# Optimization experiments

Measured on AMD Instinct MI355X. Metric: run time of the kernel, lower is better.

## Reference

```python
import jax, jax.numpy as jnp
import numpy as np

B, T, E, D, OUT = 128, 64, 256, 256, 1  # batch, timesteps, encoder_hidden, decoder_hidden, out_feats


def setup_inputs() -> dict:
    key = jax.random.key(0)
    ks = jax.random.split(key, 14)
    s = 0.05
    return {
        "input_encoded": jax.random.normal(ks[0], (B, T, E), jnp.float32),
        "y_history": jax.random.normal(ks[1], (B, T - 1, OUT), jnp.float32),
        # attn_layer: Linear(2D+E -> E), Tanh, Linear(E -> 1)
        "W_a1": jax.random.normal(ks[2], (E, 2 * D + E), jnp.float32) * s,
        "b_a1": jax.random.normal(ks[3], (E,), jnp.float32) * s,
        "W_a2": jax.random.normal(ks[4], (1, E), jnp.float32) * s,
        "b_a2": jax.random.normal(ks[5], (1,), jnp.float32) * s,
        # fc: Linear(E + out_feats -> out_feats)
        "W_fc": jax.random.normal(ks[6], (OUT, E + OUT), jnp.float32) * s,
        "b_fc": jax.random.normal(ks[7], (OUT,), jnp.float32) * s,
        # LSTM(input_size=out_feats, hidden_size=D), gate order i,f,g,o
        "W_ih": jax.random.normal(ks[8], (4 * D, OUT), jnp.float32) * s,
        "W_hh": jax.random.normal(ks[9], (4 * D, D), jnp.float32) * s,
        "b_ih": jax.random.normal(ks[10], (4 * D,), jnp.float32) * s,
        "b_hh": jax.random.normal(ks[11], (4 * D,), jnp.float32) * s,
        # fc_final: Linear(D + E -> 2) (probabilistic=True)
        "W_ff": jax.random.normal(ks[12], (2, D + E), jnp.float32) * s,
        "b_ff": jax.random.normal(ks[13], (2,), jnp.float32) * s,
    }


def reference(input_encoded, y_history, W_a1, b_a1, W_a2, b_a2, W_fc, b_fc,
              W_ih, W_hh, b_ih, b_hh, W_ff, b_ff):
    Bn, Tn, En = input_encoded.shape
    Dn = W_hh.shape[1]

    def step(carry, y_t):
        h, c, _ = carry  # h, c: [B, D]
        # concat(hidden, cell, enc) broadcast over the T encoder positions -> [B, T, 2D+E]
        feats = jnp.concatenate([
            jnp.broadcast_to(h[:, None, :], (Bn, Tn, Dn)),
            jnp.broadcast_to(c[:, None, :], (Bn, Tn, Dn)),
            input_encoded,
        ], axis=2)
        scores = jnp.tanh(feats @ W_a1.T + b_a1) @ W_a2.T + b_a2  # [B, T, 1]
        attn = jax.nn.softmax(scores[..., 0], axis=1)              # [B, T]
        context = jnp.einsum('bt,bte->be', attn, input_encoded)   # [B, E]
        y_tilde = jnp.concatenate([context, y_t], axis=1) @ W_fc.T + b_fc  # [B, 1]
        # single LSTM step, PyTorch gate order (i, f, g, o)
        gates = y_tilde @ W_ih.T + b_ih + h @ W_hh.T + b_hh       # [B, 4D]
        i, f, g, o = jnp.split(gates, 4, axis=1)
        c_new = jax.nn.sigmoid(f) * c + jax.nn.sigmoid(i) * jnp.tanh(g)
        h_new = jax.nn.sigmoid(o) * jnp.tanh(c_new)
        return (h_new, c_new, context), None

    h0 = jnp.zeros((Bn, Dn), input_encoded.dtype)
    c0 = jnp.zeros((Bn, Dn), input_encoded.dtype)
    ctx0 = jnp.zeros((Bn, En), input_encoded.dtype)
    # data_integration=True: loop runs T-1 steps over y_history
    (h, c, context), _ = jax.lax.scan(step, (h0, c0, ctx0), jnp.swapaxes(y_history, 0, 1))
    return jnp.concatenate([h, context], axis=1) @ W_ff.T + b_ff  # [B, 2]
```

## Files before the change

kernel.cpp:

```cpp
#include <hip/hip_runtime.h>
#include <math.h>

#define BATCH 128
#define TENC  64
#define NSTEP 63

#define OFF_WA1ET  0
#define OFF_EPT    65536
#define OFF_PKH    2162688
#define OFF_SX     2359296
#define OFF_HC     2375680
#define OFF_FLAGS  2441216

typedef __attribute__((ext_vector_type(8))) _Float16 h8_t;
typedef __attribute__((ext_vector_type(2))) _Float16 h2_t;

#if defined(__has_builtin)
#if __has_builtin(__builtin_amdgcn_fdot2)
#define FDOT2(a, b, c) __builtin_amdgcn_fdot2((a), (b), (c), false)
#endif
#endif
#ifndef FDOT2
#define FDOT2(a, b, c) ((c) + (float)(a)[0] * (float)(b)[0] + (float)(a)[1] * (float)(b)[1])
#endif

__device__ __forceinline__ h2_t h2of(h8_t v, int i) {
    h2_t r = {v[2 * i], v[2 * i + 1]};
    return r;
}
__device__ __forceinline__ float ftanh(float x) {
    x = fminf(15.f, fmaxf(-15.f, x));
    float e = __expf(2.f * x);
    return (e - 1.f) * __builtin_amdgcn_rcpf(e + 1.f);
}
__device__ __forceinline__ float fsig(float x) {
    return __builtin_amdgcn_rcpf(1.f + __expf(-x));
}

__global__ void pack_weights(const float* __restrict__ Wa1,
                             const float* __restrict__ Whh,
                             float* __restrict__ ws) {
    int idx = blockIdx.x * blockDim.x + threadIdx.x;
    _Float16* PKH = (_Float16*)(ws + OFF_PKH);
    if (idx < 131072) {
        int m = idx & 7, j7 = (idx >> 3) & 127, it = (idx >> 10) & 3;
        int seg = (idx >> 12) & 1, kc = (idx >> 13) & 7, hp = (idx >> 16) & 1;
        int owner = seg ? (1 - hp) : hp;
        int idx256 = kc * 32 + it * 8 + m;
        int k = (idx256 < 128) ? owner * 128 + idx256
                               : 256 + owner * 128 + (idx256 - 128);
        int j = hp * 128 + j7;
        PKH[idx] = (_Float16)Wa1[j * 768 + k];
    } else if (idx < 393216) {
        int n = idx - 131072;
        int m = n & 7, qp = (n >> 3) & 511, kh = (n >> 12) & 1, kk = (n >> 13) & 15, h1 = n >> 17;
        int q = ((qp >> 7) << 8) + h1 * 128 + (qp & 127);
        int k = kh * 128 + kk * 8 + m;
        PKH[131072 + n] = (_Float16)Whh[q * 256 + k];
    } else if (idx < 458752) {
        int n = idx - 393216;
        int k = n >> 8, j = n & 255;
        ws[OFF_WA1ET + n] = Wa1[j * 768 + 512 + k];
    }
}

__global__ void zero_flags(float* __restrict__ ws) {
    unsigned* f = (unsigned*)(ws + OFF_FLAGS);
    f[threadIdx.x] = 0u;
}

__global__ void enc_proj_kernel(const float* __restrict__ enc,
                                const float* __restrict__ ba1,
                                float* __restrict__ ws) {
    __shared__ float smem[8448];
    const int b  = blockIdx.x >> 1;
    const int th = blockIdx.x & 1;
    const int t0 = th * 32;
    const int tid = threadIdx.x;

    const float* encb = enc + (b * TENC + t0) * 256;
    for (int c = 0; c < 32; ++c) smem[c * 256 + tid] = encb[c * 256 + tid];
    __syncthreads();

    const int w = tid >> 6, l = tid & 63;
    float acc[8][4];
    #pragma unroll
    for (int a = 0; a < 8; ++a)
        #pragma unroll
        for (int c = 0; c < 4; ++c) acc[a][c] = 0.f;

    const float4* WT = (const float4*)(ws + OFF_WA1ET);
    for (int k = 0; k < 256; ++k) {
        float4 wv = WT[k * 64 + l];
        #pragma unroll
        for (int tt = 0; tt < 8; ++tt) {
            float e = smem[(w * 8 + tt) * 256 + k];
            acc[tt][0] += e * wv.x; acc[tt][1] += e * wv.y;
            acc[tt][2] += e * wv.z; acc[tt][3] += e * wv.w;
        }
    }
    float4 bb = ((const float4*)ba1)[l];
    __syncthreads();
    #pragma unroll
    for (int tt = 0; tt < 8; ++tt) {
        smem[(4 * l + 0) * 33 + w * 8 + tt] = acc[tt][0] + bb.x;
        smem[(4 * l + 1) * 33 + w * 8 + tt] = acc[tt][1] + bb.y;
        smem[(4 * l + 2) * 33 + w * 8 + tt] = acc[tt][2] + bb.z;
        smem[(4 * l + 3) * 33 + w * 8 + tt] = acc[tt][3] + bb.w;
    }
    __syncthreads();
    float* EPT = ws + OFF_EPT + b * 16384;
    for (int c = 0; c < 32; ++c) {
        int i = c * 256 + tid;
        int j = i >> 5, t5 = i & 31;
        EPT[j * 64 + t0 + t5] = smem[j * 33 + t5];
    }
}

__global__ __launch_bounds__(1024, 4) void decoder_main(
    const float* __restrict__ enc, const float* __restrict__ yhist,
    const float* __restrict__ Wa2,
    const float* __restrict__ Wfc, const float* __restrict__ bfc,
    const float* __restrict__ wih, const float* __restrict__ bih,
    const float* __restrict__ bhh,
    const float* __restrict__ Wff, const float* __restrict__ bff,
    float* __restrict__ ws, float* __restrict__ out) {

    __shared__ float hc[512];
    __shared__ _Float16 hcf16[512] __attribute__((aligned(16)));
    __shared__ float z[128];
    __shared__ float red1[1024];
    __shared__ float red2[1024];
    __shared__ float g2[1024];
    __shared__ float attnw[64];
    __shared__ float encw[64];
    __shared__ float sownl[64];
    __shared__ float wa2s[128];
    __shared__ float ys[64];
    __shared__ float ytil_s;
    __shared__ h8_t  wc[4096] __attribute__((aligned(16)));
    __shared__ float epl[8192];

    const int bid  = blockIdx.x;
    const int b    = bid & 127;
    const int h1   = bid >> 7;
    const int tid  = threadIdx.x;
    const int lane = tid & 63;
    const int wv   = tid >> 6;

    const _Float16* PKH = (const _Float16*)(ws + OFF_PKH);

    const float* EPTb = ws + OFF_EPT + b * 16384 + h1 * 8192;
    const float* encb = enc + b * 16384;
    #pragma unroll
    for (int i = 0; i < 8; ++i) epl[i * 1024 + tid] = EPTb[i * 1024 + tid];
    const h8_t* PKGown = (const h8_t*)(PKH + 131072) + h1 * 16384;
    #pragma unroll
    for (int kk = 0; kk < 4; ++kk) wc[kk * 1024 + tid] = PKGown[kk * 1024 + tid];
    if (tid < 512) { hc[tid] = 0.f; hcf16[tid] = (_Float16)0.f; }
    if (tid < 128) wa2s[tid] = Wa2[h1 * 128 + tid];
    if (tid < NSTEP) ys[tid] = yhist[b * NSTEP + tid];
    const float bfc0  = bfc[0];
    const float wfc_y = Wfc[256];
    float wii = 0.f, wif = 0.f, wig = 0.f, wio = 0.f;
    float bsi = 0.f, bsf = 0.f, bsg = 0.f, bso = 0.f;
    if (tid < 128) {
        const int q0 = h1 * 128 + tid;
        wii = wih[q0];       bsi = bih[q0]       + bhh[q0];
        wif = wih[256 + q0]; bsf = bih[256 + q0] + bhh[256 + q0];
        wig = wih[512 + q0]; bsg = bih[512 + q0] + bhh[512 + q0];
        wio = wih[768 + q0]; bso = bih[768 + q0] + bhh[768 + q0];
    }
    {
        const int t = tid >> 4, cch = tid & 15;
        float p = 0.f;
        #pragma unroll
        for (int i = 0; i < 16; ++i)
            p += encb[t * 256 + cch * 16 + i] * Wfc[cch * 16 + i];
        red1[t * 16 + cch] = p;
    }
    __syncthreads();
    if (tid < 64) {
        float s = 0.f;
        #pragma unroll
        for (int c = 0; c < 16; ++c) s += red1[tid * 16 + c];
        encw[tid] = s;
    }
    __syncthreads();

    const int kc = tid >> 7, j7 = tid & 127;
    const h8_t* W1 = (const h8_t*)PKH + h1 * 8192 + kc * 1024 + j7;
    const _Float16* hb_own  = hcf16 + ((kc < 4) ? h1 * 128 + kc * 32
                                                : 256 + h1 * 128 + (kc - 4) * 32);
    const _Float16* hb_peer = hcf16 + ((kc < 4) ? (1 - h1) * 128 + kc * 32
                                                : 256 + (1 - h1) * 128 + (kc - 4) * 32);
    const int kh = tid >> 9, qp = tid & 511;
    const h8_t* W4 = PKGown + kh * 512 + qp;
    const _Float16* hgk = hcf16 + kh * 128;

    float* SXown  = ws + OFF_SX + (b * 2 + h1) * 64;
    float* SXpeer = ws + OFF_SX + (b * 2 + (1 - h1)) * 64;
    float* HCown  = ws + OFF_HC + (b * 2 + h1) * 256;
    float* HCpeer = ws + OFF_HC + (b * 2 + (1 - h1)) * 256;
    unsigned* FLGown  = (unsigned*)(ws + OFF_FLAGS) + (b * 2 + h1) * 2;
    unsigned* FLGpeer = (unsigned*)(ws + OFF_FLAGS) + (b * 2 + (1 - h1)) * 2;

    for (int step = 0; step < NSTEP; ++step) {
        const unsigned tgt = (unsigned)(step + 1);
        float a0 = 0.f, a1 = 0.f;
        #pragma unroll
        for (int it = 0; it < 4; ++it) {
            h8_t w  = W1[it * 128];
            h8_t hv = *(const h8_t*)(hb_own + it * 8);
            a0 = FDOT2(h2of(w, 0), h2of(hv, 0), a0);
            a1 = FDOT2(h2of(w, 1), h2of(hv, 1), a1);
            a0 = FDOT2(h2of(w, 2), h2of(hv, 2), a0);
            a1 = FDOT2(h2of(w, 3), h2of(hv, 3), a1);
        }
        if (tid == 0 && step > 0) {
            while (atomicAdd(&FLGpeer[0], 0u) < (unsigned)step) { __builtin_amdgcn_s_sleep(1); }
        }
        __syncthreads();
        if (tid < 256 && step > 0) {
            float v = atomicAdd(&HCpeer[tid], 0.f);
            const int ih = (tid < 128) ? (1 - h1) * 128 + tid
                                       : 256 + (1 - h1) * 128 + (tid - 128);
            hc[ih] = v; hcf16[ih] = (_Float16)v;
        }
        __syncthreads();
        #pragma unroll
        for (int it = 0; it < 4; ++it) {
            h8_t w  = W1[512 + it * 128];
            h8_t hv = *(const h8_t*)(hb_peer + it * 8);
            a0 = FDOT2(h2of(w, 0), h2of(hv, 0), a0);
            a1 = FDOT2(h2of(w, 1), h2of(hv, 1), a1);
            a0 = FDOT2(h2of(w, 2), h2of(hv, 2), a0);
            a1 = FDOT2(h2of(w, 3), h2of(hv, 3), a1);
        }
        red1[kc * 128 + j7] = a0 + a1;
        __syncthreads();
        if (tid < 128) {
            float s = red1[tid];
            #pragma unroll
            for (int c = 1; c < 8; ++c) s += red1[c * 128 + tid];
            z[tid] = s;
        }
        __syncthreads();

        {
            const int jc = tid >> 6;
            float partial = 0.f;
            #pragma unroll
            for (int jj = 0; jj < 8; ++jj) {
                const int j = jc * 8 + jj;
                float v = epl[j * 64 + lane] + z[j];
                partial += ftanh(v) * wa2s[j];
            }
            red2[jc * 64 + lane] = partial;
        }
        __syncthreads();

        if (wv == 0) {
            float s = 0.f;
            #pragma unroll
            for (int w2 = 0; w2 < 16; ++w2) s += red2[w2 * 64 + lane];
            sownl[lane] = s;
            atomicExch(&SXown[lane], s);
            asm volatile("s_waitcnt vmcnt(0)" ::: "memory");
            if (lane == 0) atomicExch(&FLGown[1], tgt);
        }
        float g0 = 0.f, g1 = 0.f;
        #pragma unroll
        for (int kk = 0; kk < 4; ++kk) {
            h8_t w  = wc[kk * 1024 + tid];
            h8_t hv = *(const h8_t*)(hgk + kk * 8);
            g0 = FDOT2(h2of(w, 0), h2of(hv, 0), g0);
            g1 = FDOT2(h2of(w, 1), h2of(hv, 1), g1);
            g0 = FDOT2(h2of(w, 2), h2of(hv, 2), g0);
            g1 = FDOT2(h2of(w, 3), h2of(hv, 3), g1);
        }
        #pragma unroll 4
        for (int kk = 4; kk < 16; ++kk) {
            h8_t w  = W4[kk * 1024];
            h8_t hv = *(const h8_t*)(hgk + kk * 8);
            g0 = FDOT2(h2of(w, 0), h2of(hv, 0), g0);
            g1 = FDOT2(h2of(w, 1), h2of(hv, 1), g1);
            g0 = FDOT2(h2of(w, 2), h2of(hv, 2), g0);
            g1 = FDOT2(h2of(w, 3), h2of(hv, 3), g1);
        }
        g2[tid] = g0 + g1;
        if (tid == 0) {
            while (atomicAdd(&FLGpeer[1], 0u) < tgt) { __builtin_amdgcn_s_sleep(1); }
        }
        __syncthreads();

        if (wv == 0) {
            float sp = atomicAdd(&SXpeer[lane], 0.f);
            float s  = sownl[lane] + sp;
            float m = s;
            #pragma unroll
            for (int d = 32; d >= 1; d >>= 1) m = fmaxf(m, __shfl_xor(m, d));
            float e = __expf(s - m);
            float su = e;
            #pragma unroll
            for (int d = 32; d >= 1; d >>= 1) su += __shfl_xor(su, d);
            float a = e * __builtin_amdgcn_rcpf(su);
            attnw[lane] = a;
            float yp = a * encw[lane];
            #pragma unroll
            for (int d = 32; d >= 1; d >>= 1) yp += __shfl_xor(yp, d);
            if (lane == 0) ytil_s = yp + wfc_y * ys[step] + bfc0;
        }
        __syncthreads();

        if (tid < 128) {
            const float ytil = ytil_s;
            float gi = g2[tid]       + g2[512 + tid] + ytil * wii + bsi;
            float gf = g2[128 + tid] + g2[640 + tid] + ytil * wif + bsf;
            float gg = g2[256 + tid] + g2[768 + tid] + ytil * wig + bsg;
            float go = g2[384 + tid] + g2[896 + tid] + ytil * wio + bso;
            const int ih = h1 * 128 + tid;
            float co = hc[256 + ih];
            float cn = fsig(gf) * co + fsig(gi) * ftanh(gg);
            float hn = fsig(go) * ftanh(cn);
            hc[ih] = hn; hc[256 + ih] = cn;
            hcf16[ih] = (_Float16)hn; hcf16[256 + ih] = (_Float16)cn;
            atomicExch(&HCown[tid], hn);
            atomicExch(&HCown[128 + tid], cn);
        }
        __syncthreads();
        if (tid == 0) atomicExch(&FLGown[0], tgt);
    }

    if (tid == 0) {
        while (atomicAdd(&FLGpeer[0], 0u) < (unsigned)NSTEP) { __builtin_amdgcn_s_sleep(1); }
    }
    __syncthreads();
    if (tid < 128) {
        hc[(1 - h1) * 128 + tid] = atomicAdd(&HCpeer[tid], 0.f);
    }
    __syncthreads();

    if (h1 == 0) {
        if (tid < 256) {
            float cv = 0.f;
            #pragma unroll 8
            for (int t = 0; t < TENC; ++t)
                cv += attnw[t] * encb[t * 256 + tid];
            red1[tid] = cv;
        }
        __syncthreads();
        if (wv < 2) {
            float partial = 0.f;
            #pragma unroll
            for (int qq = 0; qq < 8; ++qq) {
                const int e2 = qq * 64 + lane;
                float v = (e2 < 256) ? hc[e2] : red1[e2 - 256];
                partial += v * Wff[wv * 512 + e2];
            }
            #pragma unroll
            for (int d = 32; d >= 1; d >>= 1) partial += __shfl_xor(partial, d);
            if (lane == 0) out[b * 2 + wv] = partial + bff[wv];
        }
    }
}

extern "C" void kernel_launch(void* const* d_in, const int* in_sizes, int n_in,
                              void* d_out, int out_size, void* d_ws, size_t ws_size,
                              hipStream_t stream) {
    const float* enc = (const float*)d_in[0];
    const float* yh  = (const float*)d_in[1];
    const float* Wa1 = (const float*)d_in[2];
    const float* ba1 = (const float*)d_in[3];
    const float* Wa2 = (const float*)d_in[4];
    const float* Wfc = (const float*)d_in[6];
    const float* bfc = (const float*)d_in[7];
    const float* Wih = (const float*)d_in[8];
    const float* Whh = (const float*)d_in[9];
    const float* bih = (const float*)d_in[10];
    const float* bhh = (const float*)d_in[11];
    const float* Wff = (const float*)d_in[12];
    const float* bff = (const float*)d_in[13];
    float* ws  = (float*)d_ws;
    float* out = (float*)d_out;

    hipLaunchKernelGGL(pack_weights, dim3(1792), dim3(256), 0, stream, Wa1, Whh, ws);
    hipLaunchKernelGGL(zero_flags, dim3(1), dim3(512), 0, stream, ws);
    hipLaunchKernelGGL(enc_proj_kernel, dim3(256), dim3(256), 0, stream, enc, ba1, ws);
    hipLaunchKernelGGL(decoder_main, dim3(256), dim3(1024), 0, stream,
                       enc, yh, Wa2, Wfc, bfc, Wih, bih, bhh, Wff, bff, ws, out);
}
```

Baseline: 424.2 us.

## Pack h/c exchange into fp16 pairs, cache more gate weights, drop a barrier

The cross-block exchange of h and c now packs both as fp16 into one 32-bit word, which halves the atomic global traffic per step. The two warps in the LSTM update each recompute the softmax and y_tilde themselves, so the shared scalar and one __syncthreads per step are gone. The LDS-resident portion of the recurrent weights grows from 4 to 6 chunks, which cuts global weight loads in the gate matvec. In exchange, the final h used by fc_final now carries fp16 rounding for the peer half, and the larger LDS footprint may affect occupancy.

```diff
diff --git a/kernel.cpp b/kernel.cpp
--- a/kernel.cpp
+++ b/kernel.cpp
@@ -9,8 +9,8 @@
 #define OFF_EPT    65536
 #define OFF_PKH    2162688
 #define OFF_SX     2359296
-#define OFF_HC     2375680
-#define OFF_FLAGS  2441216
+#define OFF_HX     2375680
+#define OFF_FLAGS  2408448
 
 typedef __attribute__((ext_vector_type(8))) _Float16 h8_t;
 typedef __attribute__((ext_vector_type(2))) _Float16 h2_t;
@@ -35,6 +35,11 @@
 }
 __device__ __forceinline__ float fsig(float x) {
     return __builtin_amdgcn_rcpf(1.f + __expf(-x));
+}
+__device__ __forceinline__ unsigned pack_hc(float h, float c) {
+    unsigned short hu = __builtin_bit_cast(unsigned short, (_Float16)h);
+    unsigned short cu = __builtin_bit_cast(unsigned short, (_Float16)c);
+    return (unsigned)hu | ((unsigned)cu << 16);
 }
 
 __global__ void pack_weights(const float* __restrict__ Wa1,
@@ -137,8 +142,7 @@
     __shared__ float sownl[64];
     __shared__ float wa2s[128];
     __shared__ float ys[64];
-    __shared__ float ytil_s;
-    __shared__ h8_t  wc[4096] __attribute__((aligned(16)));
+    __shared__ h8_t  wc[6144] __attribute__((aligned(16)));
     __shared__ float epl[8192];
 
     const int bid  = blockIdx.x;
@@ -156,7 +160,7 @@
     for (int i = 0; i < 8; ++i) epl[i * 1024 + tid] = EPTb[i * 1024 + tid];
     const h8_t* PKGown = (const h8_t*)(PKH + 131072) + h1 * 16384;
     #pragma unroll
-    for (int kk = 0; kk < 4; ++kk) wc[kk * 1024 + tid] = PKGown[kk * 1024 + tid];
+    for (int kk = 0; kk < 6; ++kk) wc[kk * 1024 + tid] = PKGown[kk * 1024 + tid];
     if (tid < 512) { hc[tid] = 0.f; hcf16[tid] = (_Float16)0.f; }
     if (tid < 128) wa2s[tid] = Wa2[h1 * 128 + tid];
     if (tid < NSTEP) ys[tid] = yhist[b * NSTEP + tid];
@@ -198,10 +202,10 @@
     const h8_t* W4 = PKGown + kh * 512 + qp;
     const _Float16* hgk = hcf16 + kh * 128;
 
-    float* SXown  = ws + OFF_SX + (b * 2 + h1) * 64;
-    float* SXpeer = ws + OFF_SX + (b * 2 + (1 - h1)) * 64;
-    float* HCown  = ws + OFF_HC + (b * 2 + h1) * 256;
-    float* HCpeer = ws + OFF_HC + (b * 2 + (1 - h1)) * 256;
+    float*    SXown  = ws + OFF_SX + (b * 2 + h1) * 64;
+    float*    SXpeer = ws + OFF_SX + (b * 2 + (1 - h1)) * 64;
+    unsigned* HXown  = (unsigned*)(ws + OFF_HX) + (b * 2 + h1) * 128;
+    unsigned* HXpeer = (unsigned*)(ws + OFF_HX) + (b * 2 + (1 - h1)) * 128;
     unsigned* FLGown  = (unsigned*)(ws + OFF_FLAGS) + (b * 2 + h1) * 2;
     unsigned* FLGpeer = (unsigned*)(ws + OFF_FLAGS) + (b * 2 + (1 - h1)) * 2;
 
@@ -221,11 +225,13 @@
             while (atomicAdd(&FLGpeer[0], 0u) < (unsigned)step) { __builtin_amdgcn_s_sleep(1); }
         }
         __syncthreads();
-        if (tid < 256 && step > 0) {
-            float v = atomicAdd(&HCpeer[tid], 0.f);
-            const int ih = (tid < 128) ? (1 - h1) * 128 + tid
-                                       : 256 + (1 - h1) * 128 + (tid - 128);
-            hc[ih] = v; hcf16[ih] = (_Float16)v;
+        if (tid < 128 && step > 0) {
+            unsigned u = atomicAdd(&HXpeer[tid], 0u);
+            _Float16 hv16 = __builtin_bit_cast(_Float16, (unsigned short)(u & 0xffffu));
+            _Float16 cv16 = __builtin_bit_cast(_Float16, (unsigned short)(u >> 16));
+            const int ih = (1 - h1) * 128 + tid;
+            hcf16[ih] = hv16; hcf16[256 + ih] = cv16;
+            hc[ih] = (float)hv16;
         }
         __syncthreads();
         #pragma unroll
@@ -271,7 +277,7 @@
         }
         float g0 = 0.f, g1 = 0.f;
         #pragma unroll
-        for (int kk = 0; kk < 4; ++kk) {
+        for (int kk = 0; kk < 6; ++kk) {
             h8_t w  = wc[kk * 1024 + tid];
             h8_t hv = *(const h8_t*)(hgk + kk * 8);
             g0 = FDOT2(h2of(w, 0), h2of(hv, 0), g0);
@@ -279,8 +285,8 @@
             g0 = FDOT2(h2of(w, 2), h2of(hv, 2), g0);
             g1 = FDOT2(h2of(w, 3), h2of(hv, 3), g1);
         }
-        #pragma unroll 4
-        for (int kk = 4; kk < 16; ++kk) {
+        #pragma unroll 5
+        for (int kk = 6; kk < 16; ++kk) {
             h8_t w  = W4[kk * 1024];
             h8_t hv = *(const h8_t*)(hgk + kk * 8);
             g0 = FDOT2(h2of(w, 0), h2of(hv, 0), g0);
@@ -294,7 +300,7 @@
         }
         __syncthreads();
 
-        if (wv == 0) {
+        if (tid < 128) {
             float sp = atomicAdd(&SXpeer[lane], 0.f);
             float s  = sownl[lane] + sp;
             float m = s;
@@ -305,16 +311,12 @@
             #pragma unroll
             for (int d = 32; d >= 1; d >>= 1) su += __shfl_xor(su, d);
             float a = e * __builtin_amdgcn_rcpf(su);
-            attnw[lane] = a;
+            if (wv == 0) attnw[lane] = a;
             float yp = a * encw[lane];
             #pragma unroll
             for (int d = 32; d >= 1; d >>= 1) yp += __shfl_xor(yp, d);
-            if (lane == 0) ytil_s = yp + wfc_y * ys[step] + bfc0;
-        }
-        __syncthreads();
-
-        if (tid < 128) {
-            const float ytil = ytil_s;
+            const float ytil = yp + wfc_y * ys[step] + bfc0;
+
             float gi = g2[tid]       + g2[512 + tid] + ytil * wii + bsi;
             float gf = g2[128 + tid] + g2[640 + tid] + ytil * wif + bsf;
             float gg = g2[256 + tid] + g2[768 + tid] + ytil * wig + bsg;
@@ -325,8 +327,7 @@
             float hn = fsig(go) * ftanh(cn);
             hc[ih] = hn; hc[256 + ih] = cn;
             hcf16[ih] = (_Float16)hn; hcf16[256 + ih] = (_Float16)cn;
-            atomicExch(&HCown[tid], hn);
-            atomicExch(&HCown[128 + tid], cn);
+            atomicExch(&HXown[tid], pack_hc(hn, cn));
         }
         __syncthreads();
         if (tid == 0) atomicExch(&FLGown[0], tgt);
@@ -337,7 +338,9 @@
     }
     __syncthreads();
     if (tid < 128) {
-        hc[(1 - h1) * 128 + tid] = atomicAdd(&HCpeer[tid], 0.f);
+        unsigned u = atomicAdd(&HXpeer[tid], 0u);
+        _Float16 hv16 = __builtin_bit_cast(_Float16, (unsigned short)(u & 0xffffu));
+        hc[(1 - h1) * 128 + tid] = (float)hv16;
     }
     __syncthreads();
 
```

Measured after the change: 408.4 us. -3.7%, faster.
